# Kernel optimization log

Hardware: AMD Instinct MI355X
Metric: run time of the kernel (lower is better)

The kernel has to match this reference:

```python
import jax, jax.numpy as jnp
import numpy as np

B, N, DIM = 4, 2048, 512
HEADS, DK = 8, 64
SCALE = DK ** -0.5


def setup_inputs() -> dict:
    key = jax.random.key(0)
    k1, k2, k3, k4 = jax.random.split(key, 4)
    x = jax.random.normal(k1, (B, N, DIM), dtype=jnp.float32)
    # nn.Linear(dim, dim_key*heads, bias=False): y = x @ W.T; store W already transposed
    Wq = jax.random.normal(k2, (DIM, HEADS * DK), dtype=jnp.float32) * (DIM ** -0.5)
    Wk = jax.random.normal(k3, (DIM, HEADS * DK), dtype=jnp.float32) * (DIM ** -0.5)
    rel_content_bias = jax.random.normal(k4, (1, HEADS, 1, DK), dtype=jnp.float32)
    return {"x": x, "Wq": Wq, "Wk": Wk, "rel_content_bias": rel_content_bias}


def _split_heads(t, h):
    # [b, n, h*d] -> [b, h, n, d]
    b, n, hd = t.shape
    return t.reshape(b, n, h, hd // h).transpose(0, 2, 1, 3)


def reference(x, Wq, Wk, rel_content_bias):
    q = _split_heads(x @ Wq, HEADS) * SCALE          # [b, h, n, dk]
    k = _split_heads(x @ Wk, HEADS)                  # [b, h, n, dk]
    v = _split_heads(x, HEADS)                       # [b, h, n, dim/h]
    logits = jnp.einsum('bhid,bhjd->bhij', q + rel_content_bias, k)
    attn = jax.nn.sigmoid(logits)                    # no softmax normalization
    out = jnp.einsum('bhij,bhjd->bhid', attn, v)     # [b, h, n, dim/h]
    b, h, n, d = out.shape
    return out.transpose(0, 2, 1, 3).reshape(b, n, h * d)
```

## Files before the change

### kernel.cpp

```cpp
#include <hip/hip_runtime.h>
#include <hip/hip_bf16.h>
#include <stdint.h>

#define BB 4
#define NN 2048
#define DIMD 512
#define HH 8
#define DKK 64
#define MTOT (BB * NN)
constexpr float SCALE = 0.125f;

typedef __attribute__((ext_vector_type(4))) float f32x4;
typedef __attribute__((ext_vector_type(2))) float f32x2;
typedef __attribute__((ext_vector_type(8))) short bf16x8;
typedef __attribute__((ext_vector_type(4))) _Float16 f16x4;
typedef __attribute__((ext_vector_type(2))) __fp16 fp16v2;
typedef __attribute__((ext_vector_type(4))) __fp16 fp16v4;
typedef __attribute__((ext_vector_type(2))) unsigned int u32x2;

union pack8 { unsigned short s[8]; uint4 v; };
union fragu { u32x2 h[2]; bf16x8 v; };

__device__ __forceinline__ unsigned short f2bf(float f) {
  union { float f; uint32_t u; } v; v.f = f;
  uint32_t u = v.u;
  return (unsigned short)((u + 0x7FFFu + ((u >> 16) & 1u)) >> 16);
}

__device__ __forceinline__ unsigned short f2h(float f) {
  union { _Float16 h; unsigned short u; } c; c.h = (_Float16)f;
  return c.u;
}

__device__ __forceinline__ bf16x8 ld_frag(const unsigned short* p) {
  fragu f;
  f.h[0] = *(const u32x2*)p;
  f.h[1] = *(const u32x2*)(p + 4);
  return f.v;
}
__device__ __forceinline__ void st8(unsigned short* p, uint4 v) {
  *(u32x2*)p = (u32x2){v.x, v.y};
  *(u32x2*)(p + 4) = (u32x2){v.z, v.w};
}

__device__ __forceinline__ f16x4 sig_pack(f32x4 sv) {
  float e0 = __expf(-__builtin_fabsf(sv[0]));
  float e1 = __expf(-__builtin_fabsf(sv[1]));
  float e2 = __expf(-__builtin_fabsf(sv[2]));
  float e3 = __expf(-__builtin_fabsf(sv[3]));
  const f32x2 c3 = {-0.22184f, -0.22184f};
  const f32x2 c2 = {0.66550f, 0.66550f};
  const f32x2 c1 = {-0.94280f, -0.94280f};
  const f32x2 c0 = {0.49826f, 0.49826f};
  f32x2 eA = {e0, e1}, eB = {e2, e3};
  f32x2 pA = __builtin_elementwise_fma(
      __builtin_elementwise_fma(__builtin_elementwise_fma(c3, eA, c2), eA, c1),
      eA, c0);
  f32x2 pB = __builtin_elementwise_fma(
      __builtin_elementwise_fma(__builtin_elementwise_fma(c3, eB, c2), eB, c1),
      eB, c0);
  float r0 = __builtin_copysignf(pA.x, sv[0]) + 0.5f;
  float r1 = __builtin_copysignf(pA.y, sv[1]) + 0.5f;
  float r2 = __builtin_copysignf(pB.x, sv[2]) + 0.5f;
  float r3 = __builtin_copysignf(pB.y, sv[3]) + 0.5f;
  fp16v2 lo = __builtin_amdgcn_cvt_pkrtz(r0, r1);
  fp16v2 hi = __builtin_amdgcn_cvt_pkrtz(r2, r3);
  fp16v4 p;
  p.x = lo.x; p.y = lo.y; p.z = hi.x; p.w = hi.y;
  return __builtin_bit_cast(f16x4, p);
}

__global__ __launch_bounds__(256) void prep_x(const float* __restrict__ x,
                                              unsigned short* __restrict__ xb,
                                              unsigned short* __restrict__ xtf) {
  __shared__ __align__(16) unsigned short T[64][72];
  const int b = blockIdx.z, nt = blockIdx.x, dt = blockIdx.y;
  const int tid = threadIdx.x;
  const int n0 = nt * 64, d0 = dt * 64;
  const float* src = x + ((size_t)b * NN + n0) * DIMD + d0;
#pragma unroll
  for (int r = 0; r < 2; r++) {
    int idx = tid + r * 256;
    int nl = idx >> 3, c = idx & 7;
    const float* sp = src + (size_t)nl * DIMD + c * 8;
    pack8 pb;
#pragma unroll
    for (int k = 0; k < 8; k++) {
      float f = sp[k];
      pb.s[k] = f2bf(f);
      T[c * 8 + k][nl] = f2h(f);
    }
    *(uint4*)(xb + ((size_t)b * NN + n0 + nl) * DIMD + d0 + c * 8) = pb.v;
  }
  __syncthreads();
  unsigned short* dst = xtf + ((size_t)b * DIMD + d0) * NN + n0;
#pragma unroll
  for (int r = 0; r < 2; r++) {
    int idx = tid + r * 256;
    int dl = idx >> 3, c = idx & 7;
    uint4 v = *(const uint4*)&T[dl][c * 8];
    *(uint4*)(dst + (size_t)dl * NN + c * 8) = v;
  }
}

__global__ __launch_bounds__(256) void prep_w(const float* __restrict__ wq,
                                              const float* __restrict__ wk,
                                              unsigned short* __restrict__ wtq,
                                              unsigned short* __restrict__ wtk) {
  __shared__ __align__(16) unsigned short T[64][72];
  const float* w = blockIdx.z ? wk : wq;
  unsigned short* wt = blockIdx.z ? wtk : wtq;
  const int kt = blockIdx.x, nt = blockIdx.y;
  const int tid = threadIdx.x;
  const int k0 = kt * 64, n0 = nt * 64;
#pragma unroll
  for (int r = 0; r < 16; r++) {
    int idx = tid + r * 256;
    int kl = idx >> 6, nl = idx & 63;
    T[nl][kl] = f2bf(w[(size_t)(k0 + kl) * DIMD + n0 + nl]);
  }
  __syncthreads();
#pragma unroll
  for (int r = 0; r < 2; r++) {
    int idx = tid + r * 256;
    int nl = idx >> 3, c = idx & 7;
    uint4 v = *(const uint4*)&T[nl][c * 8];
    *(uint4*)(wt + (size_t)(n0 + nl) * DIMD + k0 + c * 8) = v;
  }
}

__global__ __launch_bounds__(256) void qk_gemm(const unsigned short* __restrict__ xb,
                                               const unsigned short* __restrict__ wtq,
                                               const unsigned short* __restrict__ wtk,
                                               const float* __restrict__ bias,
                                               unsigned short* __restrict__ qout,
                                               unsigned short* __restrict__ kout) {
  __shared__ __align__(16) unsigned short Als[128][68];
  __shared__ __align__(16) unsigned short Bls[128][68];
  const int mb = blockIdx.x, nb = blockIdx.y;
  const bool isQ = (nb < 4);
  const unsigned short* wt = isQ ? wtq : wtk;
  unsigned short* outp = isQ ? qout : kout;
  const int n0 = (nb & 3) * 128, m0 = mb * 128;
  const int tid = threadIdx.x;
  const int wave = tid >> 6, lane = tid & 63;
  const int quad = lane >> 4, l16 = lane & 15;
  const int wm = wave >> 1, wn = wave & 1;

  f32x4 acc[4][4];
#pragma unroll
  for (int a = 0; a < 4; a++)
#pragma unroll
    for (int c = 0; c < 4; c++) acc[a][c] = (f32x4){0.f, 0.f, 0.f, 0.f};

  for (int k0 = 0; k0 < DIMD; k0 += 64) {
    __syncthreads();
#pragma unroll
    for (int r = 0; r < 4; r++) {
      int idx = tid + r * 256;
      int row = idx >> 3, c = idx & 7;
      st8(&Als[row][c * 8], *(const uint4*)(xb + (size_t)(m0 + row) * DIMD + k0 + c * 8));
      st8(&Bls[row][c * 8], *(const uint4*)(wt + (size_t)(n0 + row) * DIMD + k0 + c * 8));
    }
    __syncthreads();
#pragma unroll
    for (int ks = 0; ks < 2; ks++) {
      bf16x8 af[4], bfr[4];
#pragma unroll
      for (int t = 0; t < 4; t++) {
        af[t] = ld_frag(&Als[wm * 64 + t * 16 + l16][quad * 8 + ks * 32]);
        bfr[t] = ld_frag(&Bls[wn * 64 + t * 16 + l16][quad * 8 + ks * 32]);
      }
#pragma unroll
      for (int tm = 0; tm < 4; tm++)
#pragma unroll
        for (int tn = 0; tn < 4; tn++)
          acc[tm][tn] =
              __builtin_amdgcn_mfma_f32_16x16x32_bf16(af[tm], bfr[tn], acc[tm][tn], 0, 0, 0);
    }
  }
#pragma unroll
  for (int tm = 0; tm < 4; tm++) {
#pragma unroll
    for (int tn = 0; tn < 4; tn++) {
#pragma unroll
      for (int r = 0; r < 4; r++) {
        int row = m0 + wm * 64 + tm * 16 + quad * 4 + r;
        int gcol = n0 + wn * 64 + tn * 16 + l16;
        float v = acc[tm][tn][r];
        if (isQ) v = v * SCALE + bias[gcol];
        outp[(size_t)row * DIMD + gcol] = f2bf(v);
      }
    }
  }
}

__global__ __launch_bounds__(512, 4) void attn(const unsigned short* __restrict__ qb,
                                               const unsigned short* __restrict__ kb,
                                               const unsigned short* __restrict__ xtf,
                                               float* __restrict__ out) {
  __shared__ __align__(16) char smem[34816];
  unsigned short* Kbase = (unsigned short*)smem;
  unsigned short* Vbase = Kbase + 2 * 64 * 68;
  float* Obuf = (float*)smem;

  const int it = blockIdx.x, bh = blockIdx.y;
  const int b = bh >> 3, h = bh & 7;
  const int i0 = it * 128;
  const int tid = threadIdx.x;
  const int lane = tid & 63;
  const int grp = tid >> 8;
  const int wv = (tid >> 6) & 3;
  const int gtid = tid & 255;
  const int quad = lane >> 4, l16 = lane & 15;

  bf16x8 qf[2][2];
  int irow[2];
#pragma unroll
  for (int s_ = 0; s_ < 2; s_++) {
    irow[s_] = i0 + wv * 32 + s_ * 16 + l16;
    const unsigned short* qp = qb + ((size_t)b * NN + irow[s_]) * DIMD + h * DKK + quad * 8;
    qf[s_][0] = *(const bf16x8*)qp;
    qf[s_][1] = *(const bf16x8*)(qp + 32);
  }

  f32x4 o[2][4];
#pragma unroll
  for (int s_ = 0; s_ < 2; s_++)
#pragma unroll
    for (int td = 0; td < 4; td++) o[s_][td] = (f32x4){0.f, 0.f, 0.f, 0.f};

  const unsigned short* kbase = kb + (size_t)b * NN * DIMD + h * DKK;
  const unsigned short* vbase = xtf + ((size_t)b * DIMD + h * DKK) * NN;
  unsigned short* Kg = Kbase + grp * (64 * 68);
  unsigned short* Vg = Vbase + grp * (64 * 68);
  const int jbase = grp * 1024;

  for (int itr = 0; itr < 16; itr++) {
    const int j0 = jbase + itr * 64;
    __syncthreads();
#pragma unroll
    for (int r = 0; r < 2; r++) {
      int idx = gtid + r * 256;
      int row = idx >> 3, c = idx & 7;
      st8(&Kg[row * 68 + c * 8], *(const uint4*)(kbase + (size_t)(j0 + row) * DIMD + c * 8));
      st8(&Vg[row * 68 + c * 8], *(const uint4*)(vbase + (size_t)row * NN + j0 + c * 8));
    }
    __syncthreads();

#pragma unroll
    for (int t = 0; t < 4; t++) {
      bf16x8 kf0 = ld_frag(&Kg[(t * 16 + l16) * 68 + quad * 8]);
      bf16x8 kf1 = ld_frag(&Kg[(t * 16 + l16) * 68 + quad * 8 + 32]);
      f16x4 pf[2];
#pragma unroll
      for (int s_ = 0; s_ < 2; s_++) {
        f32x4 sv = (f32x4){0.f, 0.f, 0.f, 0.f};
        sv = __builtin_amdgcn_mfma_f32_16x16x32_bf16(kf0, qf[s_][0], sv, 0, 0, 0);
        sv = __builtin_amdgcn_mfma_f32_16x16x32_bf16(kf1, qf[s_][1], sv, 0, 0, 0);
        pf[s_] = sig_pack(sv);
      }
#pragma unroll
      for (int td = 0; td < 4; td++) {
        f16x4 vf = __builtin_bit_cast(
            f16x4, *(const u32x2*)&Vg[(td * 16 + l16) * 68 + t * 16 + quad * 4]);
        o[0][td] = __builtin_amdgcn_mfma_f32_16x16x16f16(vf, pf[0], o[0][td], 0, 0, 0);
        o[1][td] = __builtin_amdgcn_mfma_f32_16x16x16f16(vf, pf[1], o[1][td], 0, 0, 0);
      }
    }
  }

  __syncthreads();
  if (grp == 1) {
#pragma unroll
    for (int s_ = 0; s_ < 2; s_++)
#pragma unroll
      for (int td = 0; td < 4; td++)
        *(f32x4*)&Obuf[(wv * 32 + s_ * 16 + l16) * 68 + td * 16 + quad * 4] = o[s_][td];
  }
  __syncthreads();
  if (grp == 0) {
#pragma unroll
    for (int s_ = 0; s_ < 2; s_++) {
#pragma unroll
      for (int td = 0; td < 4; td++) {
        o[s_][td] += *(const f32x4*)&Obuf[(wv * 32 + s_ * 16 + l16) * 68 + td * 16 + quad * 4];
        float* op = out + ((size_t)b * NN + irow[s_]) * DIMD + h * DKK + td * 16 + quad * 4;
        *(f32x4*)op = o[s_][td];
      }
    }
  }
}

extern "C" void kernel_launch(void* const* d_in, const int* in_sizes, int n_in,
                              void* d_out, int out_size, void* d_ws, size_t ws_size,
                              hipStream_t stream) {
  const float* x = (const float*)d_in[0];
  const float* Wq = (const float*)d_in[1];
  const float* Wk = (const float*)d_in[2];
  const float* bias = (const float*)d_in[3];
  float* out = (float*)d_out;

  unsigned short* ws = (unsigned short*)d_ws;
  unsigned short* xb = ws;
  unsigned short* xtf = xb + (size_t)MTOT * DIMD;
  unsigned short* wtq = xtf + (size_t)MTOT * DIMD;
  unsigned short* wtk = wtq + (size_t)DIMD * DIMD;
  unsigned short* qb = wtk + (size_t)DIMD * DIMD;
  unsigned short* kb = qb + (size_t)MTOT * DIMD;

  prep_x<<<dim3(32, 8, 4), 256, 0, stream>>>(x, xb, xtf);
  prep_w<<<dim3(8, 8, 2), 256, 0, stream>>>(Wq, Wk, wtq, wtk);
  qk_gemm<<<dim3(64, 8), 256, 0, stream>>>(xb, wtq, wtk, bias, qb, kb);
  attn<<<dim3(16, 32), 512, 0, stream>>>(qb, kb, xtf, out);
}
```

Measured before the change: 159.5 us.

## Merge prep kernels and split attention key range across four wave groups

The two prep kernels become one launch that handles the x-to-bf16 cast, the transposed fp16 copy of x and the weight transpose, with simpler indexing for the transpose. The attention kernel moves from 512 to 1024 threads per block, giving four groups that each process a quarter of the key sequence. Partial outputs are then combined through a two-stage tree reduction in shared memory. This adds parallelism per query tile and saves one launch, but doubles shared memory per block, adds extra sync and reduction passes, and sets launch bounds of (1024, 8), which may force register pressure and spills.

```diff
diff --git a/kernel.cpp b/kernel.cpp
--- a/kernel.cpp
+++ b/kernel.cpp
@@ -70,62 +70,63 @@
   return __builtin_bit_cast(f16x4, p);
 }
 
-__global__ __launch_bounds__(256) void prep_x(const float* __restrict__ x,
-                                              unsigned short* __restrict__ xb,
-                                              unsigned short* __restrict__ xtf) {
-  __shared__ __align__(16) unsigned short T[64][72];
-  const int b = blockIdx.z, nt = blockIdx.x, dt = blockIdx.y;
-  const int tid = threadIdx.x;
-  const int n0 = nt * 64, d0 = dt * 64;
-  const float* src = x + ((size_t)b * NN + n0) * DIMD + d0;
-#pragma unroll
-  for (int r = 0; r < 2; r++) {
-    int idx = tid + r * 256;
-    int nl = idx >> 3, c = idx & 7;
-    const float* sp = src + (size_t)nl * DIMD + c * 8;
-    pack8 pb;
-#pragma unroll
-    for (int k = 0; k < 8; k++) {
-      float f = sp[k];
-      pb.s[k] = f2bf(f);
-      T[c * 8 + k][nl] = f2h(f);
-    }
-    *(uint4*)(xb + ((size_t)b * NN + n0 + nl) * DIMD + d0 + c * 8) = pb.v;
-  }
-  __syncthreads();
-  unsigned short* dst = xtf + ((size_t)b * DIMD + d0) * NN + n0;
-#pragma unroll
-  for (int r = 0; r < 2; r++) {
-    int idx = tid + r * 256;
-    int dl = idx >> 3, c = idx & 7;
-    uint4 v = *(const uint4*)&T[dl][c * 8];
-    *(uint4*)(dst + (size_t)dl * NN + c * 8) = v;
-  }
-}
-
-__global__ __launch_bounds__(256) void prep_w(const float* __restrict__ wq,
-                                              const float* __restrict__ wk,
-                                              unsigned short* __restrict__ wtq,
-                                              unsigned short* __restrict__ wtk) {
-  __shared__ __align__(16) unsigned short T[64][72];
-  const float* w = blockIdx.z ? wk : wq;
-  unsigned short* wt = blockIdx.z ? wtk : wtq;
-  const int kt = blockIdx.x, nt = blockIdx.y;
-  const int tid = threadIdx.x;
-  const int k0 = kt * 64, n0 = nt * 64;
-#pragma unroll
-  for (int r = 0; r < 16; r++) {
-    int idx = tid + r * 256;
-    int kl = idx >> 6, nl = idx & 63;
-    T[nl][kl] = f2bf(w[(size_t)(k0 + kl) * DIMD + n0 + nl]);
-  }
-  __syncthreads();
-#pragma unroll
-  for (int r = 0; r < 2; r++) {
-    int idx = tid + r * 256;
-    int nl = idx >> 3, c = idx & 7;
-    uint4 v = *(const uint4*)&T[nl][c * 8];
-    *(uint4*)(wt + (size_t)(n0 + nl) * DIMD + k0 + c * 8) = v;
+__global__ __launch_bounds__(256) void prep(const float* __restrict__ x,
+                                            const float* __restrict__ wq,
+                                            const float* __restrict__ wk,
+                                            unsigned short* __restrict__ xb,
+                                            unsigned short* __restrict__ xtf,
+                                            unsigned short* __restrict__ wtq,
+                                            unsigned short* __restrict__ wtk) {
+  const int bx = blockIdx.x, tid = threadIdx.x;
+  if (bx < 2048) {
+    size_t base = ((size_t)bx * 256 + tid) * 8;
+    float4 a = *(const float4*)(x + base);
+    float4 b = *(const float4*)(x + base + 4);
+    pack8 p;
+    p.s[0] = f2bf(a.x); p.s[1] = f2bf(a.y); p.s[2] = f2bf(a.z); p.s[3] = f2bf(a.w);
+    p.s[4] = f2bf(b.x); p.s[5] = f2bf(b.y); p.s[6] = f2bf(b.z); p.s[7] = f2bf(b.w);
+    *(uint4*)(xb + base) = p.v;
+  } else if (bx < 3072) {
+    int q = bx - 2048;
+    int b = q >> 8, r = q & 255;
+    int dt = r >> 5, nt = r & 31;
+    int d = dt * 64 + (tid & 63);
+    int n0 = nt * 64 + (tid >> 6) * 16;
+    const float* xp = x + ((size_t)b * NN + n0) * DIMD + d;
+    pack8 pa, pb;
+#pragma unroll
+    for (int k = 0; k < 8; k++) pa.s[k] = f2h(xp[(size_t)k * DIMD]);
+#pragma unroll
+    for (int k = 0; k < 8; k++) pb.s[k] = f2h(xp[(size_t)(k + 8) * DIMD]);
+    unsigned short* dp = xtf + ((size_t)b * DIMD + d) * NN + n0;
+    *(uint4*)dp = pa.v;
+    *(uint4*)(dp + 8) = pb.v;
+  } else {
+    __shared__ __align__(16) unsigned short T[64][68];
+    int q = bx - 3072;
+    const float* w = (q >= 64) ? wk : wq;
+    unsigned short* wt = (q >= 64) ? wtk : wtq;
+    int r = q & 63;
+    int kt = r >> 3, nt = r & 7;
+    const int k0 = kt * 64, n0 = nt * 64;
+#pragma unroll
+    for (int rr = 0; rr < 16; rr++) {
+      int idx = tid + rr * 256;
+      int kl = idx >> 6, nl = idx & 63;
+      T[nl][kl] = f2bf(w[(size_t)(k0 + kl) * DIMD + n0 + nl]);
+    }
+    __syncthreads();
+#pragma unroll
+    for (int rr = 0; rr < 2; rr++) {
+      int idx = tid + rr * 256;
+      int nl = idx >> 3, c = idx & 7;
+      fragu f;
+      f.h[0] = *(const u32x2*)&T[nl][c * 8];
+      f.h[1] = *(const u32x2*)&T[nl][c * 8 + 4];
+      uint4 v;
+      v.x = f.h[0].x; v.y = f.h[0].y; v.z = f.h[1].x; v.w = f.h[1].y;
+      *(uint4*)(wt + (size_t)(n0 + nl) * DIMD + k0 + c * 8) = v;
+    }
   }
 }
 
@@ -195,14 +196,15 @@
   }
 }
 
-__global__ __launch_bounds__(512, 4) void attn(const unsigned short* __restrict__ qb,
-                                               const unsigned short* __restrict__ kb,
-                                               const unsigned short* __restrict__ xtf,
-                                               float* __restrict__ out) {
-  __shared__ __align__(16) char smem[34816];
-  unsigned short* Kbase = (unsigned short*)smem;
-  unsigned short* Vbase = Kbase + 2 * 64 * 68;
-  float* Obuf = (float*)smem;
+__global__ __launch_bounds__(1024, 8) void attn(const unsigned short* __restrict__ qb,
+                                                const unsigned short* __restrict__ kb,
+                                                const unsigned short* __restrict__ xtf,
+                                                float* __restrict__ out) {
+  __shared__ __align__(16) char smem[69632];
+  unsigned short* Kall = (unsigned short*)smem;
+  unsigned short* Vall = Kall + 4 * 64 * 68;
+  float* R0 = (float*)smem;
+  float* R1 = R0 + 128 * 66;
 
   const int it = blockIdx.x, bh = blockIdx.y;
   const int b = bh >> 3, h = bh & 7;
@@ -232,11 +234,11 @@
 
   const unsigned short* kbase = kb + (size_t)b * NN * DIMD + h * DKK;
   const unsigned short* vbase = xtf + ((size_t)b * DIMD + h * DKK) * NN;
-  unsigned short* Kg = Kbase + grp * (64 * 68);
-  unsigned short* Vg = Vbase + grp * (64 * 68);
-  const int jbase = grp * 1024;
-
-  for (int itr = 0; itr < 16; itr++) {
+  unsigned short* Kg = Kall + grp * (64 * 68);
+  unsigned short* Vg = Vall + grp * (64 * 68);
+  const int jbase = grp * 512;
+
+  for (int itr = 0; itr < 8; itr++) {
     const int j0 = jbase + itr * 64;
     __syncthreads();
 #pragma unroll
@@ -271,12 +273,41 @@
   }
 
   __syncthreads();
-  if (grp == 1) {
+  if (grp == 1 || grp == 3) {
+    float* R = (grp == 1) ? R0 : R1;
 #pragma unroll
     for (int s_ = 0; s_ < 2; s_++)
 #pragma unroll
-      for (int td = 0; td < 4; td++)
-        *(f32x4*)&Obuf[(wv * 32 + s_ * 16 + l16) * 68 + td * 16 + quad * 4] = o[s_][td];
+      for (int td = 0; td < 4; td++) {
+        int base = (wv * 32 + s_ * 16 + l16) * 66 + td * 16 + quad * 4;
+        *(f32x2*)&R[base] = (f32x2){o[s_][td][0], o[s_][td][1]};
+        *(f32x2*)&R[base + 2] = (f32x2){o[s_][td][2], o[s_][td][3]};
+      }
+  }
+  __syncthreads();
+  if (grp == 0 || grp == 2) {
+    float* R = (grp == 0) ? R0 : R1;
+#pragma unroll
+    for (int s_ = 0; s_ < 2; s_++)
+#pragma unroll
+      for (int td = 0; td < 4; td++) {
+        int base = (wv * 32 + s_ * 16 + l16) * 66 + td * 16 + quad * 4;
+        f32x2 a = *(const f32x2*)&R[base];
+        f32x2 c = *(const f32x2*)&R[base + 2];
+        o[s_][td][0] += a.x; o[s_][td][1] += a.y;
+        o[s_][td][2] += c.x; o[s_][td][3] += c.y;
+      }
+  }
+  __syncthreads();
+  if (grp == 2) {
+#pragma unroll
+    for (int s_ = 0; s_ < 2; s_++)
+#pragma unroll
+      for (int td = 0; td < 4; td++) {
+        int base = (wv * 32 + s_ * 16 + l16) * 66 + td * 16 + quad * 4;
+        *(f32x2*)&R0[base] = (f32x2){o[s_][td][0], o[s_][td][1]};
+        *(f32x2*)&R0[base + 2] = (f32x2){o[s_][td][2], o[s_][td][3]};
+      }
   }
   __syncthreads();
   if (grp == 0) {
@@ -284,7 +315,11 @@
     for (int s_ = 0; s_ < 2; s_++) {
 #pragma unroll
       for (int td = 0; td < 4; td++) {
-        o[s_][td] += *(const f32x4*)&Obuf[(wv * 32 + s_ * 16 + l16) * 68 + td * 16 + quad * 4];
+        int base = (wv * 32 + s_ * 16 + l16) * 66 + td * 16 + quad * 4;
+        f32x2 a = *(const f32x2*)&R0[base];
+        f32x2 c = *(const f32x2*)&R0[base + 2];
+        o[s_][td][0] += a.x; o[s_][td][1] += a.y;
+        o[s_][td][2] += c.x; o[s_][td][3] += c.y;
         float* op = out + ((size_t)b * NN + irow[s_]) * DIMD + h * DKK + td * 16 + quad * 4;
         *(f32x4*)op = o[s_][td];
       }
@@ -309,8 +344,7 @@
   unsigned short* qb = wtk + (size_t)DIMD * DIMD;
   unsigned short* kb = qb + (size_t)MTOT * DIMD;
 
-  prep_x<<<dim3(32, 8, 4), 256, 0, stream>>>(x, xb, xtf);
-  prep_w<<<dim3(8, 8, 2), 256, 0, stream>>>(Wq, Wk, wtq, wtk);
+  prep<<<dim3(3200), 256, 0, stream>>>(x, Wq, Wk, xb, xtf, wtq, wtk);
   qk_gemm<<<dim3(64, 8), 256, 0, stream>>>(xb, wtq, wtk, bias, qb, kb);
-  attn<<<dim3(16, 32), 512, 0, stream>>>(qb, kb, xtf, out);
-}
+  attn<<<dim3(16, 32), 1024, 0, stream>>>(qb, kb, xtf, out);
+}
```

New measurement: 454.1 us. 185% more time.
